# Kernel tuning notes

Measured on AMD Instinct MI355X. Metric: run time of the kernel, lower is better.

The kernel has to match this reference:

```python
import jax, jax.numpy as jnp
import numpy as np

N_COARSE = 200000
M_FINE = 800000
D = 128


def setup_inputs() -> dict:
    key = jax.random.key(0)
    k1, k2 = jax.random.split(key)
    x = jax.random.normal(k1, (N_COARSE, D), dtype=jnp.float32)
    # indices into padded table: valid range [0, N_COARSE]; N_COARSE is the shadow (zero) row
    upsamples = jax.random.randint(k2, (M_FINE, 1), 0, N_COARSE + 1, dtype=jnp.int64)
    return {"x": x, "upsamples": upsamples}


def reference(x, upsamples):
    # closest_pool: pad with one zero shadow row, then gather rows by first neighbor index
    x_pad = jnp.concatenate([x, jnp.zeros_like(x[:1, :])], axis=0)  # [N+1, D]
    return x_pad[upsamples[:, 0]]  # [M, D]
```

## Files before the change

kernel.cpp:

```cpp
#include <hip/hip_runtime.h>

#define N_COARSE 200000
#define D 128
#define RPT 8

typedef float v4f __attribute__((ext_vector_type(4)));
typedef int   v4i __attribute__((ext_vector_type(4)));

__global__ void nearest_upsample_gather8(const float* __restrict__ x,
                                         const int* __restrict__ idx,
                                         float* __restrict__ out,
                                         int M) {
    int gid = blockIdx.x * blockDim.x + threadIdx.x;
    int Mg = (M + RPT - 1) / RPT;
    int total = Mg * 32;
    if (gid >= total) return;

    int g = gid >> 5;
    int c = gid & 31;

    const v4f* x4 = reinterpret_cast<const v4f*>(x);
    v4f* o4 = reinterpret_cast<v4f*>(out);
    const v4f zero = (v4f)(0.f);

    int r0 = g * RPT;

    if (r0 + RPT <= M) {
        const v4i* idx4 = reinterpret_cast<const v4i*>(idx);
        v4i jA = __builtin_nontemporal_load(idx4 + g * 2);
        v4i jB = __builtin_nontemporal_load(idx4 + g * 2 + 1);

        unsigned u[RPT] = {(unsigned)jA.x, (unsigned)jA.y, (unsigned)jA.z, (unsigned)jA.w,
                           (unsigned)jB.x, (unsigned)jB.y, (unsigned)jB.z, (unsigned)jB.w};

        v4f v[RPT];
#pragma unroll
        for (int k = 0; k < RPT; ++k) {
            unsigned kk = u[k] < N_COARSE ? u[k] : (N_COARSE - 1);
            v[k] = x4[(size_t)kk * 32 + c];
        }
#pragma unroll
        for (int k = 0; k < RPT; ++k) {
            if (u[k] >= N_COARSE) v[k] = zero;
        }

        size_t ob = (size_t)r0 * 32 + c;
#pragma unroll
        for (int k = 0; k < RPT; ++k) {
            __builtin_nontemporal_store(v[k], o4 + ob + (size_t)k * 32);
        }
    } else {
        for (int k = 0; k < RPT; ++k) {
            int r = r0 + k;
            if (r >= M) break;
            unsigned uu = (unsigned)idx[r];
            unsigned kk = uu < N_COARSE ? uu : (N_COARSE - 1);
            v4f v = x4[(size_t)kk * 32 + c];
            if (uu >= N_COARSE) v = zero;
            __builtin_nontemporal_store(v, o4 + (size_t)r * 32 + c);
        }
    }
}

extern "C" void kernel_launch(void* const* d_in, const int* in_sizes, int n_in,
                              void* d_out, int out_size, void* d_ws, size_t ws_size,
                              hipStream_t stream) {
    const float* x = (const float*)d_in[0];
    const int* idx = (const int*)d_in[1];
    float* out = (float*)d_out;

    int M = in_sizes[1];
    int Mg = (M + RPT - 1) / RPT;
    int total = Mg * 32;
    int block = 256;
    int grid = (total + block - 1) / block;

    nearest_upsample_gather8<<<grid, block, 0, stream>>>(x, idx, out, M);
}
```

Measured before the change: 118.0 us.

## Split gather into source-row chunks across multiple kernel launches for cache locality

Replaces the single gather launch with eight launches. Each launch copies only the output rows whose index falls in one slice of the source table, so the table slice being read (about 12.8 MB) can stay in cache. The cost is that every launch rereads the full index array and scans every output row, adds kernel launch overhead, and turns the writes into scattered, branch-dependent stores. The tail-handling path is merged into a bounds check inside the loop.

```diff
diff --git a/kernel.cpp b/kernel.cpp
--- a/kernel.cpp
+++ b/kernel.cpp
@@ -3,14 +3,16 @@
 #define N_COARSE 200000
 #define D 128
 #define RPT 8
+#define NCHUNK 8
+#define CHUNK_ROWS ((N_COARSE + NCHUNK - 1) / NCHUNK)
 
 typedef float v4f __attribute__((ext_vector_type(4)));
 typedef int   v4i __attribute__((ext_vector_type(4)));
 
-__global__ void nearest_upsample_gather8(const float* __restrict__ x,
-                                         const int* __restrict__ idx,
-                                         float* __restrict__ out,
-                                         int M) {
+__global__ void nearest_upsample_chunk(const float* __restrict__ x,
+                                       const int* __restrict__ idx,
+                                       float* __restrict__ out,
+                                       int M, int lo, int hi, int first) {
     int gid = blockIdx.x * blockDim.x + threadIdx.x;
     int Mg = (M + RPT - 1) / RPT;
     int total = Mg * 32;
@@ -24,40 +26,21 @@
     const v4f zero = (v4f)(0.f);
 
     int r0 = g * RPT;
+    const v4i* idx4 = reinterpret_cast<const v4i*>(idx);
+    v4i jA = idx4[(size_t)g * 2];
+    v4i jB = idx4[(size_t)g * 2 + 1];
+    int u[RPT] = {jA.x, jA.y, jA.z, jA.w, jB.x, jB.y, jB.z, jB.w};
 
-    if (r0 + RPT <= M) {
-        const v4i* idx4 = reinterpret_cast<const v4i*>(idx);
-        v4i jA = __builtin_nontemporal_load(idx4 + g * 2);
-        v4i jB = __builtin_nontemporal_load(idx4 + g * 2 + 1);
-
-        unsigned u[RPT] = {(unsigned)jA.x, (unsigned)jA.y, (unsigned)jA.z, (unsigned)jA.w,
-                           (unsigned)jB.x, (unsigned)jB.y, (unsigned)jB.z, (unsigned)jB.w};
-
-        v4f v[RPT];
+    size_t ob = (size_t)r0 * 32 + c;
 #pragma unroll
-        for (int k = 0; k < RPT; ++k) {
-            unsigned kk = u[k] < N_COARSE ? u[k] : (N_COARSE - 1);
-            v[k] = x4[(size_t)kk * 32 + c];
-        }
-#pragma unroll
-        for (int k = 0; k < RPT; ++k) {
-            if (u[k] >= N_COARSE) v[k] = zero;
-        }
-
-        size_t ob = (size_t)r0 * 32 + c;
-#pragma unroll
-        for (int k = 0; k < RPT; ++k) {
-            __builtin_nontemporal_store(v[k], o4 + ob + (size_t)k * 32);
-        }
-    } else {
-        for (int k = 0; k < RPT; ++k) {
-            int r = r0 + k;
-            if (r >= M) break;
-            unsigned uu = (unsigned)idx[r];
-            unsigned kk = uu < N_COARSE ? uu : (N_COARSE - 1);
-            v4f v = x4[(size_t)kk * 32 + c];
-            if (uu >= N_COARSE) v = zero;
-            __builtin_nontemporal_store(v, o4 + (size_t)r * 32 + c);
+    for (int k = 0; k < RPT; ++k) {
+        if (r0 + k >= M) break;
+        int uk = u[k];
+        if (uk >= lo && uk < hi) {
+            v4f v = x4[(size_t)uk * 32 + c];
+            __builtin_nontemporal_store(v, o4 + ob + (size_t)k * 32);
+        } else if (first && (unsigned)uk >= (unsigned)N_COARSE) {
+            __builtin_nontemporal_store(zero, o4 + ob + (size_t)k * 32);
         }
     }
 }
@@ -75,5 +58,11 @@
     int block = 256;
     int grid = (total + block - 1) / block;
 
-    nearest_upsample_gather8<<<grid, block, 0, stream>>>(x, idx, out, M);
+    for (int chunk = 0; chunk < NCHUNK; ++chunk) {
+        int lo = chunk * CHUNK_ROWS;
+        int hi = lo + CHUNK_ROWS;
+        if (hi > N_COARSE) hi = N_COARSE;
+        nearest_upsample_chunk<<<grid, block, 0, stream>>>(
+            x, idx, out, M, lo, hi, chunk == 0 ? 1 : 0);
+    }
 }
```

Result: slower. 158.8 us (+34.6%).
